# Kernel tuning notes

Measured on AMD Instinct MI355X. Metric: run time of the kernel, lower is better.

The kernel has to match this reference:

```python
import jax, jax.numpy as jnp
import numpy as np

B, T, H, E, V, S, L = 64, 512, 256, 128, 32000, 128, 16


def setup_inputs() -> dict:
    key = jax.random.key(0)
    ks = jax.random.split(key, 12)
    f = lambda k, shp, s: jax.random.normal(k, shp, dtype=jnp.float32) * s
    return {
        "u_enc_out": f(ks[0], (T, B, H), 0.1),
        "last_hidden": f(ks[1], (1, B, H), 0.1),
        "z_tm1": jax.random.randint(ks[2], (1, B), 0, V),
        "slot_vocab_map": jax.random.randint(ks[3], (L, S), 0, V),
        "emb_W": f(ks[4], (V, E), 0.02),
        "emb_ctrl_W": f(ks[5], (E, E), 0.05),
        "emb_ctrl_b": jnp.zeros((E,), jnp.float32),
        "attn_W": f(ks[6], (H, 2 * H), 0.05),
        "attn_b": jnp.zeros((H,), jnp.float32),
        "attn_v": f(ks[7], (H,), 1.0 / np.sqrt(H).astype(np.float32)),
        "ffnn_hidden_W": f(ks[8], (H, 2 * H + E), 0.05),
        "ffnn_hidden_b": jnp.zeros((H,), jnp.float32),
        "ffnn_out_W": f(ks[9], (S, H), 0.05),
        "ffnn_out_b": jnp.zeros((S,), jnp.float32),
    }


def reference(u_enc_out, last_hidden, z_tm1, slot_vocab_map, emb_W, emb_ctrl_W,
              emb_ctrl_b, attn_W, attn_b, attn_v, ffnn_hidden_W, ffnn_hidden_b,
              ffnn_out_W, ffnn_out_b):
    # --- Bahdanau additive attention (Attn.forward, pv_z_enc_out is None) ---
    enc = u_enc_out.transpose(1, 0, 2)                      # [B,T,H]
    b, t, h = enc.shape
    h_rep = jnp.broadcast_to(last_hidden.transpose(1, 0, 2), (b, t, h))
    energy = jnp.tanh(jnp.concatenate([h_rep, enc], axis=-1) @ attn_W.T + attn_b)  # [B,T,H]
    scores = jnp.einsum('bth,h->bt', energy, attn_v)        # [B,T]
    w = jax.nn.softmax(scores, axis=1)
    context = jnp.einsum('bt,bth->bh', w, enc)[None]        # [1,B,H]
    # --- embedding + control projection (dropout_rate = 0.0) ---
    embed_z = emb_W[z_tm1]                                  # [1,B,E]
    embed_z = embed_z + (embed_z @ emb_ctrl_W.T + emb_ctrl_b)
    # --- FFNN ---
    ffnn_in = jnp.concatenate([embed_z, context, last_hidden], axis=-1)  # [1,B,2H+E]
    hidden = jax.nn.relu(ffnn_in @ ffnn_hidden_W.T + ffnn_hidden_b)      # [1,B,H]
    gen_score = jax.nn.relu(hidden @ ffnn_out_W.T + ffnn_out_b)[0]       # [B,S]
    # --- scatter-add vocab mapping: replaces the nested Python loop ---
    vocab_size = emb_W.shape[0]

    def per_step(cols):  # cols: [S] int token ids (duplicates accumulate)
        full = jnp.full((gen_score.shape[0], vocab_size), -0.01, gen_score.dtype)
        full = full.at[:, cols].add(gen_score)
        return jax.nn.softmax(full, axis=1)

    probas = jax.vmap(per_step)(slot_vocab_map)             # [L,B,V]
    return hidden, probas
```

## Files before the change

kernel.cpp:

```cpp
#include <hip/hip_runtime.h>
#include <hip/hip_bf16.h>

#define BB 64
#define TT 512
#define HH 256
#define EE 128
#define VV 32000
#define SS 128
#define LL 16

typedef __attribute__((ext_vector_type(8))) short bf16x8;
typedef __attribute__((ext_vector_type(4))) float f32x4;

static __device__ __forceinline__ unsigned short f2bf(float x) {
    unsigned int u = __float_as_uint(x);
    unsigned int r = (u + 0x7fffu + ((u >> 16) & 1u)) >> 16;
    return (unsigned short)r;
}

static __device__ __forceinline__ float ftanh(float x) {
    float y = __builtin_amdgcn_exp2f(x * 2.885390082f);
    return 1.f - 2.f * __builtin_amdgcn_rcpf(y + 1.f);
}

__global__ __launch_bounds__(256) void k_pre(const float* __restrict__ last_hidden,
                                             const float* __restrict__ attn_W,
                                             const float* __restrict__ attn_b,
                                             const int* __restrict__ z_tm1,
                                             const float* __restrict__ emb_W,
                                             const float* __restrict__ ctrl_W,
                                             const float* __restrict__ ctrl_b,
                                             const int* __restrict__ slot,
                                             float* __restrict__ hW,
                                             float* __restrict__ embed,
                                             unsigned short* __restrict__ Bs,
                                             int* __restrict__ fidx) {
    __shared__ float sh[HH];
    __shared__ int shi[256];
    int blk = blockIdx.x;
    int tid = threadIdx.x;
    if (blk < 64) {
        int b = blk, h = tid;
        sh[h] = last_hidden[b * HH + h];
        __syncthreads();
        const float4* wrow = (const float4*)(attn_W + (size_t)h * (2 * HH));
        float a0 = 0.f, a1 = 0.f, a2 = 0.f, a3 = 0.f;
        for (int k4 = 0; k4 < HH / 4; k4 += 4) {
            float4 w0 = wrow[k4], w1 = wrow[k4+1], w2 = wrow[k4+2], w3 = wrow[k4+3];
            a0 += sh[k4*4+ 0]*w0.x + sh[k4*4+ 1]*w0.y + sh[k4*4+ 2]*w0.z + sh[k4*4+ 3]*w0.w;
            a1 += sh[k4*4+ 4]*w1.x + sh[k4*4+ 5]*w1.y + sh[k4*4+ 6]*w1.z + sh[k4*4+ 7]*w1.w;
            a2 += sh[k4*4+ 8]*w2.x + sh[k4*4+ 9]*w2.y + sh[k4*4+10]*w2.z + sh[k4*4+11]*w2.w;
            a3 += sh[k4*4+12]*w3.x + sh[k4*4+13]*w3.y + sh[k4*4+14]*w3.z + sh[k4*4+15]*w3.w;
        }
        hW[b * HH + h] = attn_b[h] + ((a0 + a1) + (a2 + a3));
    } else if (blk < 96) {
        int idx = (blk - 64) * 256 + tid;
        int lane = idx & 63;
        int gt = (idx >> 6) & 15;
        int ks = idx >> 10;
        int col = gt * 16 + (lane & 15);
        int k0 = ks * 32 + (lane >> 4) * 8;
        const float* src = attn_W + (size_t)col * (2 * HH) + HH + k0;
        unsigned int p0 = f2bf(src[0]) | ((unsigned int)f2bf(src[1]) << 16);
        unsigned int p1 = f2bf(src[2]) | ((unsigned int)f2bf(src[3]) << 16);
        unsigned int p2 = f2bf(src[4]) | ((unsigned int)f2bf(src[5]) << 16);
        unsigned int p3 = f2bf(src[6]) | ((unsigned int)f2bf(src[7]) << 16);
        *(uint4*)(Bs + (size_t)idx * 8) = make_uint4(p0, p1, p2, p3);
    } else if (blk < 160) {
        int b = blk - 96;
        if (tid < EE) sh[tid] = emb_W[(size_t)z_tm1[b] * EE + tid];
        __syncthreads();
        if (tid < EE) {
            const float4* wrow = (const float4*)(ctrl_W + (size_t)tid * EE);
            float a0 = 0.f, a1 = 0.f;
            for (int k4 = 0; k4 < EE / 4; k4 += 2) {
                float4 w0 = wrow[k4], w1 = wrow[k4+1];
                a0 += sh[k4*4+0]*w0.x + sh[k4*4+1]*w0.y + sh[k4*4+2]*w0.z + sh[k4*4+3]*w0.w;
                a1 += sh[k4*4+4]*w1.x + sh[k4*4+5]*w1.y + sh[k4*4+6]*w1.z + sh[k4*4+7]*w1.w;
            }
            embed[b * EE + tid] = ctrl_b[tid] + sh[tid] + a0 + a1;
        }
    } else {
        int lblk = (blk - 160) * 2;
        shi[tid] = slot[lblk * SS + tid];
        __syncthreads();
        int lrow = tid >> 7, s = tid & 127;
        int c = shi[lrow * 128 + s];
        int fi = s;
        for (int s2 = 0; s2 < 128; ++s2) {
            if (shi[lrow * 128 + s2] == c) { fi = s2; break; }
        }
        fidx[(lblk + lrow) * SS + s] = fi;
    }
}

__global__ __launch_bounds__(256) void k_sctx(const float* __restrict__ enc,
                                              const unsigned short* __restrict__ Bs,
                                              const float* __restrict__ attn_v,
                                              const float* __restrict__ hW,
                                              float* __restrict__ partial,
                                              float* __restrict__ mArr,
                                              float* __restrict__ dArr) {
    __shared__ uint4 AbufV[1024];
    __shared__ float scpart[128];
    __shared__ float wloc[32];
    __shared__ __align__(16) float part[1024];
    unsigned char* Abuf = (unsigned char*)AbufV;

    int c = blockIdx.x, b = blockIdx.y;
    int tid = threadIdx.x;
    int t0 = c * 32;

#pragma unroll
    for (int it = 0; it < 4; ++it) {
        int ci = tid + it * 256;
        int row = ci >> 5;
        int kc = ci & 31;
        const float* src = enc + ((size_t)(t0 + row) * BB + b) * HH + kc * 8;
        float4 f0 = *(const float4*)src;
        float4 f1 = *(const float4*)(src + 4);
        unsigned int p0 = f2bf(f0.x) | ((unsigned int)f2bf(f0.y) << 16);
        unsigned int p1 = f2bf(f0.z) | ((unsigned int)f2bf(f0.w) << 16);
        unsigned int p2 = f2bf(f1.x) | ((unsigned int)f2bf(f1.y) << 16);
        unsigned int p3 = f2bf(f1.z) | ((unsigned int)f2bf(f1.w) << 16);
        int addr = (row * 512 + kc * 16) ^ ((row & 7) << 4);
        *(uint4*)(Abuf + addr) = make_uint4(p0, p1, p2, p3);
    }
    __syncthreads();

    int wv = tid >> 6, lane = tid & 63;
    int lrow = lane & 15, q = lane >> 4;

    f32x4 acc[2][4];
#pragma unroll
    for (int rt = 0; rt < 2; ++rt)
#pragma unroll
        for (int ct = 0; ct < 4; ++ct) acc[rt][ct] = (f32x4){0.f, 0.f, 0.f, 0.f};

    const bf16x8* BsV = (const bf16x8*)Bs;
    for (int ks = 0; ks < 8; ++ks) {
        bf16x8 bfr[4];
        const bf16x8* bsrc = BsV + ((size_t)(ks * 16 + wv * 4) * 64 + lane);
#pragma unroll
        for (int ct = 0; ct < 4; ++ct) bfr[ct] = bsrc[ct * 64];
        bf16x8 afr[2];
#pragma unroll
        for (int rt = 0; rt < 2; ++rt) {
            int arow = rt * 16 + lrow;
            int abyte = (arow * 512 + ks * 64 + q * 16) ^ ((arow & 7) << 4);
            afr[rt] = *(const bf16x8*)(Abuf + abyte);
        }
#pragma unroll
        for (int rt = 0; rt < 2; ++rt)
#pragma unroll
            for (int ct = 0; ct < 4; ++ct)
                acc[rt][ct] = __builtin_amdgcn_mfma_f32_16x16x32_bf16(afr[rt], bfr[ct], acc[rt][ct], 0, 0, 0);
    }

    float vvv[4], hwv[4];
#pragma unroll
    for (int ct = 0; ct < 4; ++ct) {
        int col = wv * 64 + ct * 16 + lrow;
        vvv[ct] = attn_v[col];
        hwv[ct] = hW[(size_t)b * HH + col];
    }
#pragma unroll
    for (int rt = 0; rt < 2; ++rt) {
        float ps[4];
#pragma unroll
        for (int r = 0; r < 4; ++r) {
            float s = 0.f;
#pragma unroll
            for (int ct = 0; ct < 4; ++ct)
                s += vvv[ct] * ftanh(acc[rt][ct][r] + hwv[ct]);
#pragma unroll
            for (int off = 1; off < 16; off <<= 1) s += __shfl_xor(s, off, 64);
            ps[r] = s;
        }
        if (lrow == 0) {
#pragma unroll
            for (int r = 0; r < 4; ++r) scpart[wv * 32 + rt * 16 + q * 4 + r] = ps[r];
        }
    }
    __syncthreads();

    if (tid < 64) {
        float s = (tid < 32)
            ? ((scpart[tid] + scpart[32 + tid]) + (scpart[64 + tid] + scpart[96 + tid]))
            : -3.0e38f;
        float mx = s;
#pragma unroll
        for (int off = 32; off; off >>= 1) mx = fmaxf(mx, __shfl_xor(mx, off, 64));
        float e = (tid < 32) ? expf(s - mx) : 0.f;
        float d = e;
#pragma unroll
        for (int off = 32; off; off >>= 1) d += __shfl_xor(d, off, 64);
        if (tid < 32) wloc[tid] = e;
        if (tid == 0) { mArr[b * 16 + c] = mx; dArr[b * 16 + c] = d; }
    }
    __syncthreads();

    {
        int h4 = tid & 63, g = tid >> 6;
        f32x4 c4 = {0.f, 0.f, 0.f, 0.f};
        f32x4 d4 = {0.f, 0.f, 0.f, 0.f};
        const f32x4* enc4 = (const f32x4*)enc;
        size_t base = ((size_t)(t0 + g * 8) * BB + b) * 64 + h4;
#pragma unroll
        for (int i = 0; i < 8; i += 2) {
            float w0 = wloc[g * 8 + i], w1 = wloc[g * 8 + i + 1];
            f32x4 v0 = enc4[base + (size_t)i * BB * 64];
            f32x4 v1 = enc4[base + (size_t)(i + 1) * BB * 64];
            c4.x += w0 * v0.x; c4.y += w0 * v0.y; c4.z += w0 * v0.z; c4.w += w0 * v0.w;
            d4.x += w1 * v1.x; d4.y += w1 * v1.y; d4.z += w1 * v1.z; d4.w += w1 * v1.w;
        }
        c4.x += d4.x; c4.y += d4.y; c4.z += d4.z; c4.w += d4.w;
        *(f32x4*)&part[g * 256 + h4 * 4] = c4;
    }
    __syncthreads();
    if (tid < 64) {
        f32x4 a0 = *(const f32x4*)&part[0 * 256 + tid * 4];
        f32x4 a1 = *(const f32x4*)&part[1 * 256 + tid * 4];
        f32x4 a2 = *(const f32x4*)&part[2 * 256 + tid * 4];
        f32x4 a3 = *(const f32x4*)&part[3 * 256 + tid * 4];
        f32x4 t4;
        t4.x = (a0.x + a1.x) + (a2.x + a3.x);
        t4.y = (a0.y + a1.y) + (a2.y + a3.y);
        t4.z = (a0.z + a1.z) + (a2.z + a3.z);
        t4.w = (a0.w + a1.w) + (a2.w + a3.w);
        *(f32x4*)&partial[((size_t)c * BB + b) * HH + tid * 4] = t4;
    }
}

__global__ __launch_bounds__(256) void k_fin(const float* __restrict__ partial,
                                             const float* __restrict__ mArr,
                                             const float* __restrict__ dArr,
                                             const float* __restrict__ embed,
                                             const float* __restrict__ last_hidden,
                                             float* __restrict__ fin) {
    __shared__ float ldm[16], ldd[16];
    int b = blockIdx.x, tid = threadIdx.x;
    if (tid < 16) { ldm[tid] = mArr[b * 16 + tid]; ldd[tid] = dArr[b * 16 + tid]; }
    __syncthreads();
    float M = ldm[0];
#pragma unroll
    for (int c = 1; c < 16; ++c) M = fmaxf(M, ldm[c]);
    float den = 0.f;
#pragma unroll
    for (int c = 0; c < 16; ++c) den += expf(ldm[c] - M) * ldd[c];
    float invden = 1.f / den;
    float esc[16];
#pragma unroll
    for (int c = 0; c < 16; ++c) esc[c] = expf(ldm[c] - M) * invden;

    for (int j = tid; j < 2 * HH + EE; j += 256) {
        float v;
        if (j < EE) v = embed[b * EE + j];
        else if (j < EE + HH) {
            int h = j - EE;
            float a0 = 0.f, a1 = 0.f;
#pragma unroll
            for (int c = 0; c < 16; c += 2) {
                a0 += esc[c]     * partial[(size_t)c * BB * HH + b * HH + h];
                a1 += esc[c + 1] * partial[(size_t)(c + 1) * BB * HH + b * HH + h];
            }
            v = a0 + a1;
        } else v = last_hidden[b * HH + (j - EE - HH)];
        fin[b * 640 + j] = v;
    }
}

__global__ __launch_bounds__(256) void k_hid(const float* __restrict__ fin,
                                             const float* __restrict__ Whid,
                                             float* __restrict__ paccum) {
    __shared__ __align__(16) float W_sl[8 * 80];
    __shared__ float fin_sl[64 * 81];
    int og = blockIdx.x >> 3, kg = blockIdx.x & 7;
    int tid = threadIdx.x;
    int k0 = kg * 80, o0 = og * 8;

    for (int i = tid; i < 8 * 80; i += 256) {
        int o = i / 80, kk = i - o * 80;
        W_sl[i] = Whid[(size_t)(o0 + o) * 640 + k0 + kk];
    }
    {
        int b = tid & 63, kc = tid >> 6;
#pragma unroll
        for (int j = 0; j < 20; ++j) {
            int kk = kc * 20 + j;
            fin_sl[b * 81 + kk] = fin[b * 640 + k0 + kk];
        }
    }
    __syncthreads();

    int b = tid & 63, g = tid >> 6;
    float a0 = 0.f, a1 = 0.f;
    for (int kk = 0; kk < 80; kk += 4) {
        f32x4 w0 = *(const f32x4*)&W_sl[(g * 2) * 80 + kk];
        f32x4 w1 = *(const f32x4*)&W_sl[(g * 2 + 1) * 80 + kk];
        float f0 = fin_sl[b * 81 + kk + 0];
        float f1 = fin_sl[b * 81 + kk + 1];
        float f2 = fin_sl[b * 81 + kk + 2];
        float f3 = fin_sl[b * 81 + kk + 3];
        a0 += f0 * w0.x + f1 * w0.y + f2 * w0.z + f3 * w0.w;
        a1 += f0 * w1.x + f1 * w1.y + f2 * w1.z + f3 * w1.w;
    }
    paccum[kg * 16384 + b * 256 + o0 + g * 2 + 0] = a0;
    paccum[kg * 16384 + b * 256 + o0 + g * 2 + 1] = a1;
}

__global__ __launch_bounds__(256) void k_gensum(const float* __restrict__ paccum,
                                                const float* __restrict__ bhid,
                                                const float* __restrict__ Wout,
                                                const float* __restrict__ bout,
                                                float* __restrict__ out_hidden,
                                                float* __restrict__ gen) {
    __shared__ __align__(16) float WoutL[4 * 256];
    __shared__ float hid_ld[8 * 257];
    __shared__ float boutL[4];
    int sg = blockIdx.x >> 3, bh = blockIdx.x & 7;
    int tid = threadIdx.x;
    int b0 = bh * 8;

    for (int i = tid; i < 4 * 256; i += 256)
        WoutL[i] = Wout[(size_t)(sg * 4 + (i >> 8)) * HH + (i & 255)];
    if (tid < 4) boutL[tid] = bout[sg * 4 + tid];

#pragma unroll
    for (int it = 0; it < 8; ++it) {
        int bidx = (b0 + it) * 256 + tid;
        float v = ((paccum[0 * 16384 + bidx] + paccum[1 * 16384 + bidx])
                 + (paccum[2 * 16384 + bidx] + paccum[3 * 16384 + bidx]))
                + ((paccum[4 * 16384 + bidx] + paccum[5 * 16384 + bidx])
                 + (paccum[6 * 16384 + bidx] + paccum[7 * 16384 + bidx]))
                + bhid[tid];
        hid_ld[it * 257 + tid] = fmaxf(v, 0.f);
    }
    __syncthreads();

    if (sg == 0) {
#pragma unroll
        for (int it = 0; it < 8; ++it)
            out_hidden[(size_t)(b0 + it) * HH + tid] = hid_ld[it * 257 + tid];
    }

    {
        int oi = tid >> 3, kt = tid & 7;
        int sq = oi >> 3, bq = oi & 7;
        float acc = 0.f;
#pragma unroll 8
        for (int jj = 0; jj < 32; ++jj) {
            int k = kt * 32 + ((jj + 4 * kt) & 31);
            acc += hid_ld[bq * 257 + k] * WoutL[sq * 256 + k];
        }
        acc += __shfl_xor(acc, 1, 64);
        acc += __shfl_xor(acc, 2, 64);
        acc += __shfl_xor(acc, 4, 64);
        if (kt == 0)
            gen[(size_t)(b0 + bq) * SS + sg * 4 + sq] = fmaxf(acc + boutL[sq], 0.f);
    }
}

__global__ __launch_bounds__(256) void k_fill(const int* __restrict__ slot,
                                              const int* __restrict__ fidx,
                                              const float* __restrict__ gen,
                                              float* __restrict__ out) {
    __shared__ float genl[SS], genacc[SS], pv[SS];
    __shared__ float red[12];
    __shared__ int fidxL[SS], cls[SS];
    int bx = blockIdx.x;
    int row = bx >> 1, half = bx & 1;
    int l = row >> 6, b = row & 63;
    int tid = threadIdx.x;
    int lane = tid & 63, wv = tid >> 6;

    if (tid < SS) {
        genl[tid] = gen[(size_t)b * SS + tid];
        fidxL[tid] = fidx[l * SS + tid];
        cls[tid] = slot[l * SS + tid];
        genacc[tid] = 0.f;
    }
    __syncthreads();
    if (tid < SS) atomicAdd(&genacc[fidxL[tid]], genl[tid]);
    __syncthreads();

    float mg = 0.f;
    bool first = false;
    if (tid < SS) {
        first = (fidxL[tid] == tid);
        mg = -0.01f + genacc[tid];
    }
    float mx = first ? mg : -3.0e38f;
#pragma unroll
    for (int off = 32; off; off >>= 1) mx = fmaxf(mx, __shfl_xor(mx, off, 64));
    if (lane == 0) red[wv] = mx;
    __syncthreads();
    float M = fmaxf(red[0], red[1]);
    float e = first ? expf(mg - M) : 0.f;
    float s1 = e, s2 = first ? 1.f : 0.f;
#pragma unroll
    for (int off = 32; off; off >>= 1) {
        s1 += __shfl_xor(s1, off, 64);
        s2 += __shfl_xor(s2, off, 64);
    }
    if (lane == 0) { red[4 + wv] = s1; red[8 + wv] = s2; }
    __syncthreads();
    float sumHits = red[4] + red[5];
    float cntv = red[8] + red[9];
    float base = expf(-0.01f - M);
    float inv = 1.f / (((float)VV - cntv) * base + sumHits);
    float pb = base * inv;
    if (tid < SS) pv[tid] = first ? e * inv : -1.f;
    __syncthreads();

    float* rowp = out + BB * HH + ((size_t)(l * BB + b)) * VV;
    float4 p4 = make_float4(pb, pb, pb, pb);
    float4* row4 = (float4*)rowp + half * (VV / 8);
#pragma unroll 4
    for (int idx = tid; idx < VV / 8; idx += 256) row4[idx] = p4;
    __syncthreads();
    if (tid < SS && pv[tid] >= 0.f) {
        int c = cls[tid];
        int lo = half * (VV / 2);
        if (c >= lo && c < lo + VV / 2) rowp[c] = pv[tid];
    }
}

extern "C" void kernel_launch(void* const* d_in, const int* in_sizes, int n_in,
                              void* d_out, int out_size, void* d_ws, size_t ws_size,
                              hipStream_t stream) {
    const float* u_enc       = (const float*)d_in[0];
    const float* last_hidden = (const float*)d_in[1];
    const int*   z_tm1       = (const int*)d_in[2];
    const int*   slot        = (const int*)d_in[3];
    const float* emb_W       = (const float*)d_in[4];
    const float* ctrl_W      = (const float*)d_in[5];
    const float* ctrl_b      = (const float*)d_in[6];
    const float* attn_W      = (const float*)d_in[7];
    const float* attn_b      = (const float*)d_in[8];
    const float* attn_v      = (const float*)d_in[9];
    const float* Whid        = (const float*)d_in[10];
    const float* bhid        = (const float*)d_in[11];
    const float* Wout        = (const float*)d_in[12];
    const float* bout        = (const float*)d_in[13];
    float* out = (float*)d_out;
    float* ws = (float*)d_ws;

    float* mArr    = ws;
    float* dArr    = ws + 1024;
    float* hW      = ws + 32768;
    float* embed   = ws + 49152;
    float* gen     = ws + 57344;
    unsigned short* Bs = (unsigned short*)(ws + 65536);
    float* partial = ws + 98304;
    float* fin     = ws + 360448;
    float* paccum  = ws + 401408;
    int*   fidx    = (int*)(ws + 532480);

    k_pre<<<168, 256, 0, stream>>>(last_hidden, attn_W, attn_b, z_tm1, emb_W, ctrl_W,
                                   ctrl_b, slot, hW, embed, Bs, fidx);
    dim3 gs(16, BB);
    k_sctx<<<gs, 256, 0, stream>>>(u_enc, Bs, attn_v, hW, partial, mArr, dArr);
    k_fin<<<BB, 256, 0, stream>>>(partial, mArr, dArr, embed, last_hidden, fin);
    k_hid<<<256, 256, 0, stream>>>(fin, Whid, paccum);
    k_gensum<<<256, 256, 0, stream>>>(paccum, bhid, Wout, bout, out, gen);
    k_fill<<<LL * BB * 2, 256, 0, stream>>>(slot, fidx, gen, out);
}
```

Before: 65.65 us.

## Split-K hidden projection, reuse bf16 LDS tile for context, widen fin grid

Splits the last_hidden·attn_W projection into two K-halves across 128 blocks, writing partial sums that the attention kernel adds together. The context accumulation now reads the bf16 encoder tile already staged in LDS instead of re-reading fp32 encoder rows from global memory. The partial layout is changed to batch-major, and the final gather kernel runs four blocks per batch row. This removes the second global pass over the encoder and adds parallelism to the small prep kernels, at the cost of bf16 precision in the context sum.

```diff
diff --git a/kernel.cpp b/kernel.cpp
--- a/kernel.cpp
+++ b/kernel.cpp
@@ -31,7 +31,7 @@
                                              const float* __restrict__ ctrl_W,
                                              const float* __restrict__ ctrl_b,
                                              const int* __restrict__ slot,
-                                             float* __restrict__ hW,
+                                             float* __restrict__ hWp,
                                              float* __restrict__ embed,
                                              unsigned short* __restrict__ Bs,
                                              int* __restrict__ fidx) {
@@ -39,22 +39,22 @@
     __shared__ int shi[256];
     int blk = blockIdx.x;
     int tid = threadIdx.x;
-    if (blk < 64) {
-        int b = blk, h = tid;
-        sh[h] = last_hidden[b * HH + h];
+    if (blk < 128) {
+        int b = blk >> 1, kh = blk & 1;
+        if (tid < 128) sh[tid] = last_hidden[b * HH + kh * 128 + tid];
         __syncthreads();
-        const float4* wrow = (const float4*)(attn_W + (size_t)h * (2 * HH));
-        float a0 = 0.f, a1 = 0.f, a2 = 0.f, a3 = 0.f;
-        for (int k4 = 0; k4 < HH / 4; k4 += 4) {
-            float4 w0 = wrow[k4], w1 = wrow[k4+1], w2 = wrow[k4+2], w3 = wrow[k4+3];
-            a0 += sh[k4*4+ 0]*w0.x + sh[k4*4+ 1]*w0.y + sh[k4*4+ 2]*w0.z + sh[k4*4+ 3]*w0.w;
-            a1 += sh[k4*4+ 4]*w1.x + sh[k4*4+ 5]*w1.y + sh[k4*4+ 6]*w1.z + sh[k4*4+ 7]*w1.w;
-            a2 += sh[k4*4+ 8]*w2.x + sh[k4*4+ 9]*w2.y + sh[k4*4+10]*w2.z + sh[k4*4+11]*w2.w;
-            a3 += sh[k4*4+12]*w3.x + sh[k4*4+13]*w3.y + sh[k4*4+14]*w3.z + sh[k4*4+15]*w3.w;
-        }
-        hW[b * HH + h] = attn_b[h] + ((a0 + a1) + (a2 + a3));
-    } else if (blk < 96) {
-        int idx = (blk - 64) * 256 + tid;
+        const float4* wrow = (const float4*)(attn_W + (size_t)tid * (2 * HH) + kh * 128);
+        float a0 = 0.f, a1 = 0.f;
+        for (int k4 = 0; k4 < 32; k4 += 2) {
+            float4 w0 = wrow[k4], w1 = wrow[k4 + 1];
+            a0 += sh[k4*4+0]*w0.x + sh[k4*4+1]*w0.y + sh[k4*4+2]*w0.z + sh[k4*4+3]*w0.w;
+            a1 += sh[k4*4+4]*w1.x + sh[k4*4+5]*w1.y + sh[k4*4+6]*w1.z + sh[k4*4+7]*w1.w;
+        }
+        float r = a0 + a1;
+        if (kh == 0) r += attn_b[tid];
+        hWp[kh * 16384 + b * 256 + tid] = r;
+    } else if (blk < 160) {
+        int idx = (blk - 128) * 256 + tid;
         int lane = idx & 63;
         int gt = (idx >> 6) & 15;
         int ks = idx >> 10;
@@ -66,22 +66,22 @@
         unsigned int p2 = f2bf(src[4]) | ((unsigned int)f2bf(src[5]) << 16);
         unsigned int p3 = f2bf(src[6]) | ((unsigned int)f2bf(src[7]) << 16);
         *(uint4*)(Bs + (size_t)idx * 8) = make_uint4(p0, p1, p2, p3);
-    } else if (blk < 160) {
-        int b = blk - 96;
+    } else if (blk < 224) {
+        int b = blk - 160;
         if (tid < EE) sh[tid] = emb_W[(size_t)z_tm1[b] * EE + tid];
         __syncthreads();
         if (tid < EE) {
             const float4* wrow = (const float4*)(ctrl_W + (size_t)tid * EE);
             float a0 = 0.f, a1 = 0.f;
             for (int k4 = 0; k4 < EE / 4; k4 += 2) {
-                float4 w0 = wrow[k4], w1 = wrow[k4+1];
+                float4 w0 = wrow[k4], w1 = wrow[k4 + 1];
                 a0 += sh[k4*4+0]*w0.x + sh[k4*4+1]*w0.y + sh[k4*4+2]*w0.z + sh[k4*4+3]*w0.w;
                 a1 += sh[k4*4+4]*w1.x + sh[k4*4+5]*w1.y + sh[k4*4+6]*w1.z + sh[k4*4+7]*w1.w;
             }
             embed[b * EE + tid] = ctrl_b[tid] + sh[tid] + a0 + a1;
         }
     } else {
-        int lblk = (blk - 160) * 2;
+        int lblk = (blk - 224) * 2;
         shi[tid] = slot[lblk * SS + tid];
         __syncthreads();
         int lrow = tid >> 7, s = tid & 127;
@@ -97,7 +97,7 @@
 __global__ __launch_bounds__(256) void k_sctx(const float* __restrict__ enc,
                                               const unsigned short* __restrict__ Bs,
                                               const float* __restrict__ attn_v,
-                                              const float* __restrict__ hW,
+                                              const float* __restrict__ hWp,
                                               float* __restrict__ partial,
                                               float* __restrict__ mArr,
                                               float* __restrict__ dArr) {
@@ -162,7 +162,7 @@
     for (int ct = 0; ct < 4; ++ct) {
         int col = wv * 64 + ct * 16 + lrow;
         vvv[ct] = attn_v[col];
-        hwv[ct] = hW[(size_t)b * HH + col];
+        hwv[ct] = hWp[(size_t)b * HH + col] + hWp[16384 + (size_t)b * HH + col];
     }
 #pragma unroll
     for (int rt = 0; rt < 2; ++rt) {
@@ -202,20 +202,22 @@
 
     {
         int h4 = tid & 63, g = tid >> 6;
-        f32x4 c4 = {0.f, 0.f, 0.f, 0.f};
-        f32x4 d4 = {0.f, 0.f, 0.f, 0.f};
-        const f32x4* enc4 = (const f32x4*)enc;
-        size_t base = ((size_t)(t0 + g * 8) * BB + b) * 64 + h4;
-#pragma unroll
-        for (int i = 0; i < 8; i += 2) {
-            float w0 = wloc[g * 8 + i], w1 = wloc[g * 8 + i + 1];
-            f32x4 v0 = enc4[base + (size_t)i * BB * 64];
-            f32x4 v1 = enc4[base + (size_t)(i + 1) * BB * 64];
-            c4.x += w0 * v0.x; c4.y += w0 * v0.y; c4.z += w0 * v0.z; c4.w += w0 * v0.w;
-            d4.x += w1 * v1.x; d4.y += w1 * v1.y; d4.z += w1 * v1.z; d4.w += w1 * v1.w;
-        }
-        c4.x += d4.x; c4.y += d4.y; c4.z += d4.z; c4.w += d4.w;
-        *(f32x4*)&part[g * 256 + h4 * 4] = c4;
+        float c0 = 0.f, c1 = 0.f, c2 = 0.f, c3 = 0.f;
+#pragma unroll
+        for (int i = 0; i < 8; ++i) {
+            int row = g * 8 + i;
+            float wt = wloc[row];
+            int baddr = ((row * 512 + (h4 >> 1) * 16) ^ ((row & 7) << 4)) + (h4 & 1) * 8;
+            ushort4 u = *(const ushort4*)(Abuf + baddr);
+            c0 += wt * __uint_as_float((unsigned int)u.x << 16);
+            c1 += wt * __uint_as_float((unsigned int)u.y << 16);
+            c2 += wt * __uint_as_float((unsigned int)u.z << 16);
+            c3 += wt * __uint_as_float((unsigned int)u.w << 16);
+        }
+        part[g * 256 + h4 * 4 + 0] = c0;
+        part[g * 256 + h4 * 4 + 1] = c1;
+        part[g * 256 + h4 * 4 + 2] = c2;
+        part[g * 256 + h4 * 4 + 3] = c3;
     }
     __syncthreads();
     if (tid < 64) {
@@ -228,7 +230,7 @@
         t4.y = (a0.y + a1.y) + (a2.y + a3.y);
         t4.z = (a0.z + a1.z) + (a2.z + a3.z);
         t4.w = (a0.w + a1.w) + (a2.w + a3.w);
-        *(f32x4*)&partial[((size_t)c * BB + b) * HH + tid * 4] = t4;
+        *(f32x4*)&partial[((size_t)b * 16 + c) * HH + tid * 4] = t4;
     }
 }
 
@@ -239,7 +241,8 @@
                                              const float* __restrict__ last_hidden,
                                              float* __restrict__ fin) {
     __shared__ float ldm[16], ldd[16];
-    int b = blockIdx.x, tid = threadIdx.x;
+    int b = blockIdx.x >> 2, qq = blockIdx.x & 3;
+    int tid = threadIdx.x;
     if (tid < 16) { ldm[tid] = mArr[b * 16 + tid]; ldd[tid] = dArr[b * 16 + tid]; }
     __syncthreads();
     float M = ldm[0];
@@ -249,22 +252,21 @@
 #pragma unroll
     for (int c = 0; c < 16; ++c) den += expf(ldm[c] - M) * ldd[c];
     float invden = 1.f / den;
-    float esc[16];
-#pragma unroll
-    for (int c = 0; c < 16; ++c) esc[c] = expf(ldm[c] - M) * invden;
-
-    for (int j = tid; j < 2 * HH + EE; j += 256) {
+
+    int j = qq * 160 + tid;
+    if (tid < 160) {
         float v;
         if (j < EE) v = embed[b * EE + j];
         else if (j < EE + HH) {
             int h = j - EE;
+            const float* pb = partial + (size_t)b * 16 * HH + h;
             float a0 = 0.f, a1 = 0.f;
 #pragma unroll
             for (int c = 0; c < 16; c += 2) {
-                a0 += esc[c]     * partial[(size_t)c * BB * HH + b * HH + h];
-                a1 += esc[c + 1] * partial[(size_t)(c + 1) * BB * HH + b * HH + h];
+                a0 += expf(ldm[c] - M) * pb[(size_t)c * HH];
+                a1 += expf(ldm[c + 1] - M) * pb[(size_t)(c + 1) * HH];
             }
-            v = a0 + a1;
+            v = (a0 + a1) * invden;
         } else v = last_hidden[b * HH + (j - EE - HH)];
         fin[b * 640 + j] = v;
     }
@@ -448,20 +450,20 @@
 
     float* mArr    = ws;
     float* dArr    = ws + 1024;
-    float* hW      = ws + 32768;
-    float* embed   = ws + 49152;
-    float* gen     = ws + 57344;
-    unsigned short* Bs = (unsigned short*)(ws + 65536);
-    float* partial = ws + 98304;
-    float* fin     = ws + 360448;
-    float* paccum  = ws + 401408;
-    int*   fidx    = (int*)(ws + 532480);
-
-    k_pre<<<168, 256, 0, stream>>>(last_hidden, attn_W, attn_b, z_tm1, emb_W, ctrl_W,
-                                   ctrl_b, slot, hW, embed, Bs, fidx);
+    float* hWp     = ws + 2048;
+    float* embed   = ws + 34816;
+    float* gen     = ws + 43008;
+    unsigned short* Bs = (unsigned short*)(ws + 51200);
+    float* partial = ws + 83968;
+    float* fin     = ws + 346112;
+    float* paccum  = ws + 387072;
+    int*   fidx    = (int*)(ws + 518144);
+
+    k_pre<<<232, 256, 0, stream>>>(last_hidden, attn_W, attn_b, z_tm1, emb_W, ctrl_W,
+                                   ctrl_b, slot, hWp, embed, Bs, fidx);
     dim3 gs(16, BB);
-    k_sctx<<<gs, 256, 0, stream>>>(u_enc, Bs, attn_v, hW, partial, mArr, dArr);
-    k_fin<<<BB, 256, 0, stream>>>(partial, mArr, dArr, embed, last_hidden, fin);
+    k_sctx<<<gs, 256, 0, stream>>>(u_enc, Bs, attn_v, hWp, partial, mArr, dArr);
+    k_fin<<<BB * 4, 256, 0, stream>>>(partial, mArr, dArr, embed, last_hidden, fin);
     k_hid<<<256, 256, 0, stream>>>(fin, Whid, paccum);
     k_gensum<<<256, 256, 0, stream>>>(paccum, bhid, Wout, bout, out, gen);
     k_fill<<<LL * BB * 2, 256, 0, stream>>>(slot, fidx, gen, out);
```

New measurement: 64.15 us (median of 2 runs). 2.3% less time.
